# Performance work log

Hardware: AMD Instinct MI355X
Metric: run time of the kernel (lower is better)

## Reference

```python
import jax, jax.numpy as jnp
import numpy as np
import math

D_MODEL = 1024
N_HEADS = 16
D_K = D_MODEL // N_HEADS
D_FF = 4096
B, S = 4, 2048
EPS = 1e-5


def setup_inputs() -> dict:
    key = jax.random.key(0)
    ks = jax.random.split(key, 16)
    def xav(k, shape):
        fan_in, fan_out = shape[0], shape[1]
        lim = math.sqrt(6.0 / (fan_in + fan_out))
        return jax.random.uniform(k, shape, jnp.float32, -lim, lim)
    return {
        "query": jax.random.normal(ks[0], (B, S, D_MODEL), jnp.float32),
        "key": jax.random.normal(ks[1], (B, S, D_MODEL), jnp.float32),
        "values": jax.random.normal(ks[2], (B, S, D_MODEL), jnp.float32),
        # weights stored (in, out) so y = x @ W + b (transpose of torch layout)
        "Wk": xav(ks[3], (D_MODEL, D_MODEL)), "bk": jnp.zeros((D_MODEL,)),
        "Wv": xav(ks[4], (D_MODEL, D_MODEL)), "bv": jnp.zeros((D_MODEL,)),
        "Wout": xav(ks[5], (D_MODEL, D_MODEL)), "bout": jnp.zeros((D_MODEL,)),
        "gammas": jax.random.normal(ks[6], (N_HEADS, 1, 1), jnp.float32) * 0.5,
        "ln1_s": jnp.ones((D_MODEL,)), "ln1_b": jnp.zeros((D_MODEL,)),
        "W1": xav(ks[7], (D_MODEL, D_FF)), "b1": jnp.zeros((D_FF,)),
        "W2": xav(ks[8], (D_FF, D_MODEL)), "b2": jnp.zeros((D_MODEL,)),
        "ln2_s": jnp.ones((D_MODEL,)), "ln2_b": jnp.zeros((D_MODEL,)),
    }


def _layernorm(x, scale, bias):
    mu = jnp.mean(x, axis=-1, keepdims=True)
    var = jnp.mean((x - mu) ** 2, axis=-1, keepdims=True)
    return (x - mu) * jax.lax.rsqrt(var + EPS) * scale + bias


def reference(query, key, values, Wk, bk, Wv, bv, Wout, bout, gammas,
              ln1_s, ln1_b, W1, b1, W2, b2, ln2_s, ln2_b):
    bs, seqlen, _ = query.shape
    # NOTE: original code projects q with k_linear (shared weights) - kept faithful.
    q = (query @ Wk + bk).reshape(bs, seqlen, N_HEADS, D_K).transpose(0, 2, 1, 3)
    k = (key @ Wk + bk).reshape(bs, seqlen, N_HEADS, D_K).transpose(0, 2, 1, 3)
    v = (values @ Wv + bv).reshape(bs, seqlen, N_HEADS, D_K).transpose(0, 2, 1, 3)

    scores = jnp.einsum("bhqd,bhkd->bhqk", q, k) / math.sqrt(D_K)  # [B,H,S,S]

    idx = jnp.arange(seqlen)
    position_effect = jnp.abs(idx[None, :] - idx[:, None]).astype(jnp.float32) / 21.0  # [S,S]
    gamma = -jax.nn.softplus(gammas)  # [H,1,1]
    # exp(-pos * gamma) = exp(pos * softplus(gammas)), clamped to [1e-5, 1e5]
    total_effect = jnp.clip(jnp.exp(-position_effect[None, :, :] * gamma), 1e-5, 1e5)  # [H,S,S]
    scores = scores * total_effect[None]

    causal = jnp.tril(jnp.ones((seqlen, seqlen), dtype=bool))  # allowed positions
    scores = jnp.where(causal[None, None], scores, -1e32)
    att_weight = jax.nn.softmax(scores, axis=-1)  # dropout is identity (eval)

    ctx = jnp.einsum("bhqk,bhkd->bhqd", att_weight, v)
    concat = ctx.transpose(0, 2, 1, 3).reshape(bs, seqlen, D_MODEL)
    attn_out = concat @ Wout + bout

    x = _layernorm(query + attn_out, ln1_s, ln1_b)
    ffn = jax.nn.relu(x @ W1 + b1) @ W2 + b2
    x = _layernorm(x + ffn, ln2_s, ln2_b)
    return (x, att_weight)
```

## Files before the change

kernel.cpp:

```cpp
#include <hip/hip_runtime.h>
#include <math.h>

typedef unsigned short u16;
typedef float f32x4 __attribute__((ext_vector_type(4)));
typedef short s16x8 __attribute__((ext_vector_type(8)));

#define D_MODEL 1024
#define NH 16
#define DK 64
#define DFF 4096
#define BB 4
#define SS 2048
#define ROWS (BB*SS)
#define MiB 1048576ull
#define BHSZ 4194304ull
#define QKS  131072ull

static __device__ __forceinline__ float bf2f(u16 v){
  union{unsigned u; float f;} x; x.u = ((unsigned)v)<<16; return x.f;
}
static __device__ __forceinline__ u16 f2bf(float f){
  union{float f; unsigned u;} x; x.f=f;
  unsigned r = x.u + 0x7fffu + ((x.u>>16)&1u);
  return (u16)(r>>16);
}
static __device__ __forceinline__ double softplus64(float gf){
  double g = (double)gf;
  return (g > 0.0) ? g + log1p(exp(-g)) : log1p(exp(g));
}

__global__ __launch_bounds__(256) void twc(const float* __restrict__ in,
    u16* __restrict__ oh, u16* __restrict__ om, u16* __restrict__ ol, int R, int C){
  __shared__ float t[32][33];
  int c0 = blockIdx.x*32, r0 = blockIdx.y*32;
  int tx = threadIdx.x & 31, ty = threadIdx.x >> 5;
  for (int i=ty; i<32; i+=8) t[i][tx] = in[(size_t)(r0+i)*C + c0 + tx];
  __syncthreads();
  for (int i=ty; i<32; i+=8){
    float x = t[tx][i];
    u16 h = f2bf(x);
    size_t o = (size_t)(c0+i)*R + r0 + tx;
    oh[o] = h;
    if (om){
      float r1 = x - bf2f(h);
      u16 m = f2bf(r1);
      om[o] = m;
      if (ol){ float r2 = r1 - bf2f(m); ol[o] = f2bf(r2); }
    }
  }
}

__global__ __launch_bounds__(256) void copyf(float* __restrict__ dst,
                                             const float* __restrict__ src, long long n){
  long long i = (long long)blockIdx.x*256 + threadIdx.x;
  long long stride = (long long)gridDim.x*256;
  for (; i < n; i += stride) dst[i] = src[i];
}

__global__ __launch_bounds__(256) void gemm3(
    const float* __restrict__ A, const u16* __restrict__ Bh,
    const u16* __restrict__ Bm, const u16* __restrict__ Bl,
    const float* __restrict__ bias, int M, int N, int K, int kt, float* __restrict__ o)
{
  __shared__ u16 lAh[128*32], lAm[128*32], lAl[128*32];
  __shared__ u16 lBh[128*32], lBm[128*32], lBl[128*32];
  const int tid = threadIdx.x, wid = tid>>6, L = tid&63;
  const int m0 = blockIdx.y*128, n0 = blockIdx.x*128;
  const int wm = (wid>>1)*64, wn = (wid&1)*64;
  f32x4 acc[4][4] = {};
  const int srow = wid*32 + (L>>2);
  const int scol = (L&3)*8;
  for (int ktile=0; ktile<K; ktile+=32){
    s16x8 ah[2], am[2], al[2], vbh[2], vbm[2], vbl[2];
    #pragma unroll
    for (int rr=0; rr<2; rr++){
      const float* ap = &A[(size_t)(m0 + srow + rr*16)*K + ktile + scol];
      #pragma unroll
      for (int e=0;e<8;e++){
        float x = ap[e];
        u16 hh = f2bf(x); float r1 = x - bf2f(hh);
        u16 mm = f2bf(r1); float r2 = r1 - bf2f(mm);
        ah[rr][e] = (short)hh; am[rr][e] = (short)mm; al[rr][e] = (short)f2bf(r2);
      }
      const size_t bo = (size_t)(n0 + srow + rr*16)*K + ktile + scol;
      vbh[rr] = *(const s16x8*)&Bh[bo];
      vbm[rr] = *(const s16x8*)&Bm[bo];
      vbl[rr] = *(const s16x8*)&Bl[bo];
    }
    __syncthreads();
    #pragma unroll
    for (int rr=0; rr<2; rr++){
      const int ro = (srow + rr*16)*32 + scol;
      *(s16x8*)&lAh[ro] = ah[rr]; *(s16x8*)&lAm[ro] = am[rr]; *(s16x8*)&lAl[ro] = al[rr];
      *(s16x8*)&lBh[ro] = vbh[rr]; *(s16x8*)&lBm[ro] = vbm[rr]; *(s16x8*)&lBl[ro] = vbl[rr];
    }
    __syncthreads();
    const int lro = (L&15)*32 + (L>>4)*8;
    s16x8 afh[4], afm[4], afl[4], bfh[4], bfm[4], bfl[4];
    #pragma unroll
    for (int t=0;t<4;t++){
      afh[t] = *(const s16x8*)&lAh[(wm + t*16)*32 + lro];
      afm[t] = *(const s16x8*)&lAm[(wm + t*16)*32 + lro];
      afl[t] = *(const s16x8*)&lAl[(wm + t*16)*32 + lro];
      bfh[t] = *(const s16x8*)&lBh[(wn + t*16)*32 + lro];
      bfm[t] = *(const s16x8*)&lBm[(wn + t*16)*32 + lro];
      bfl[t] = *(const s16x8*)&lBl[(wn + t*16)*32 + lro];
    }
    #pragma unroll
    for (int mt=0;mt<4;mt++)
      #pragma unroll
      for (int nt=0;nt<4;nt++){
        f32x4 a2 = acc[mt][nt];
        a2 = __builtin_amdgcn_mfma_f32_16x16x32_bf16(afl[mt], bfh[nt], a2, 0,0,0);
        a2 = __builtin_amdgcn_mfma_f32_16x16x32_bf16(afm[mt], bfm[nt], a2, 0,0,0);
        a2 = __builtin_amdgcn_mfma_f32_16x16x32_bf16(afh[mt], bfl[nt], a2, 0,0,0);
        a2 = __builtin_amdgcn_mfma_f32_16x16x32_bf16(afm[mt], bfh[nt], a2, 0,0,0);
        a2 = __builtin_amdgcn_mfma_f32_16x16x32_bf16(afh[mt], bfm[nt], a2, 0,0,0);
        a2 = __builtin_amdgcn_mfma_f32_16x16x32_bf16(afh[mt], bfh[nt], a2, 0,0,0);
        acc[mt][nt] = a2;
      }
  }
  #pragma unroll
  for (int mt=0;mt<4;mt++)
    #pragma unroll
    for (int nt=0;nt<4;nt++){
      const int gn = n0 + wn + nt*16 + (L&15);
      const float bvv = bias[gn];
      const int gmb = m0 + wm + mt*16 + (L>>4)*4;
      const int h = gn>>6, d = gn&63;
      #pragma unroll
      for (int r=0;r<4;r++){
        const int gm = gmb + r, b = gm>>11, s = gm&2047;
        const float v = acc[mt][nt][r] + bvv;
        if (kt) o[((size_t)(b*NH+h)*DK + d)*SS + s] = v;
        else    o[((size_t)(b*NH+h)*SS + s)*DK + d] = v;
      }
    }
}

__global__ __launch_bounds__(256) void gemm2(
    const float* __restrict__ A, const u16* __restrict__ Bh, const u16* __restrict__ Bl,
    const float* __restrict__ bias, int M, int N, int K, int mode, float* __restrict__ o)
{
  __shared__ u16 lAh[128*32], lAl[128*32], lBh[128*32], lBl[128*32];
  const int tid = threadIdx.x, wid = tid>>6, L = tid&63;
  const int m0 = blockIdx.y*128, n0 = blockIdx.x*128;
  const int wm = (wid>>1)*64, wn = (wid&1)*64;
  f32x4 acc[4][4] = {};
  const int srow = wid*32 + (L>>2);
  const int scol = (L&3)*8;
  for (int kt=0; kt<K; kt+=32){
    s16x8 ah[2], al[2], vbh[2], vbl[2];
    #pragma unroll
    for (int rr=0; rr<2; rr++){
      const float* ap = &A[(size_t)(m0 + srow + rr*16)*K + kt + scol];
      #pragma unroll
      for (int e=0;e<8;e++){
        float x = ap[e];
        u16 hh = f2bf(x);
        ah[rr][e] = (short)hh;
        al[rr][e] = (short)f2bf(x - bf2f(hh));
      }
      const size_t bo = (size_t)(n0 + srow + rr*16)*K + kt + scol;
      vbh[rr] = *(const s16x8*)&Bh[bo];
      vbl[rr] = *(const s16x8*)&Bl[bo];
    }
    __syncthreads();
    #pragma unroll
    for (int rr=0; rr<2; rr++){
      const int ro = (srow + rr*16)*32 + scol;
      *(s16x8*)&lAh[ro] = ah[rr]; *(s16x8*)&lAl[ro] = al[rr];
      *(s16x8*)&lBh[ro] = vbh[rr]; *(s16x8*)&lBl[ro] = vbl[rr];
    }
    __syncthreads();
    const int lro = (L&15)*32 + (L>>4)*8;
    s16x8 afh[4], afl[4], bfh[4], bfl[4];
    #pragma unroll
    for (int t=0;t<4;t++){
      afh[t] = *(const s16x8*)&lAh[(wm + t*16)*32 + lro];
      afl[t] = *(const s16x8*)&lAl[(wm + t*16)*32 + lro];
      bfh[t] = *(const s16x8*)&lBh[(wn + t*16)*32 + lro];
      bfl[t] = *(const s16x8*)&lBl[(wn + t*16)*32 + lro];
    }
    #pragma unroll
    for (int mt=0;mt<4;mt++)
      #pragma unroll
      for (int nt=0;nt<4;nt++){
        f32x4 a2 = acc[mt][nt];
        a2 = __builtin_amdgcn_mfma_f32_16x16x32_bf16(afl[mt], bfh[nt], a2, 0,0,0);
        a2 = __builtin_amdgcn_mfma_f32_16x16x32_bf16(afh[mt], bfl[nt], a2, 0,0,0);
        a2 = __builtin_amdgcn_mfma_f32_16x16x32_bf16(afh[mt], bfh[nt], a2, 0,0,0);
        acc[mt][nt] = a2;
      }
  }
  #pragma unroll
  for (int mt=0;mt<4;mt++)
    #pragma unroll
    for (int nt=0;nt<4;nt++){
      const int gn = n0 + wn + nt*16 + (L&15);
      const float bvv = bias[gn];
      const int gmb = m0 + wm + mt*16 + (L>>4)*4;
      #pragma unroll
      for (int r=0;r<4;r++){
        const int gm = gmb + r;
        float v = acc[mt][nt][r] + bvv;
        if (mode==0)      o[(size_t)gm*N + gn] = v;
        else if (mode==1) o[(size_t)gm*N + gn] = fmaxf(v, 0.f);
        else {
          const int b = gm>>11, s = gm&2047, h = gn>>6, d = gn&63;
          o[((size_t)(b*NH+h)*SS + s)*DK + d] = v;
        }
      }
    }
}

__global__ __launch_bounds__(256) void attn_row(
  const float* __restrict__ q, const float* __restrict__ k, long long qs,
  int bh0, int row0,
  const float* __restrict__ vb, const float* __restrict__ gammas,
  float* __restrict__ att, float* __restrict__ ctx,
  int aw_lo, int aw_hi, int wc)
{
  __shared__ float  sqf[64][4];
  __shared__ float  p4[1024*4];
  __shared__ double red[4][4];
  __shared__ float  cpart[4][4][64];
  const int i0 = row0 + blockIdx.x*4;
  const int i3 = i0 + 3;
  const int bh = bh0 + blockIdx.y, h = bh&15, b = bh>>4;
  const int wa = (bh >= aw_lo) && (bh < aw_hi);
  const int t = threadIdx.x, wid = t>>6, L = t&63;
  const double c = softplus64(gammas[h]) * (1.0/21.0);

  {
    const int r = t>>6, d = t&63;
    sqf[d][r] = q[(size_t)blockIdx.y*qs + (size_t)(i0+r)*DK + d];
  }
  const double ce1   = exp(-c);
  const double er    = exp(c);
  const double tstep = exp(-1024.0 * c);
  double u0 = exp(c * (double)(i0 - 4*t));
  double err1 = er, err2 = er*er, err3 = err2*er;
  __syncthreads();

  const float* kb = k + (size_t)blockIdx.y*qs;
  double sv[4][8];
  double lmax[4] = {-1e300,-1e300,-1e300,-1e300};
  #pragma unroll
  for (int tile=0; tile<2; tile++){
    const int j0 = tile*1024 + 4*t;
    if (j0 <= i3){
      const float* kcol = kb + j0;
      double acc[4][4];
      #pragma unroll
      for (int r=0;r<4;r++)
        #pragma unroll
        for (int e=0;e<4;e++) acc[r][e] = 0.0;
      #pragma unroll 4
      for (int d=0; d<64; d++){
        f32x4 kv = *(const f32x4*)(kcol + (size_t)d*SS);
        f32x4 qv = *(const f32x4*)&sqf[d][0];
        const double k0=(double)kv[0], k1=(double)kv[1];
        const double k2=(double)kv[2], k3=(double)kv[3];
        #pragma unroll
        for (int r=0;r<4;r++){
          const double qd = (double)qv[r];
          acc[r][0] = fma(k0, qd, acc[r][0]);
          acc[r][1] = fma(k1, qd, acc[r][1]);
          acc[r][2] = fma(k2, qd, acc[r][2]);
          acc[r][3] = fma(k3, qd, acc[r][3]);
        }
      }
      #pragma unroll
      for (int r=0;r<4;r++){
        double uu = u0 * ((r==0)?1.0:(r==1)?err1:(r==2)?err2:err3);
        const int ir = i0 + r;
        #pragma unroll
        for (int e=0;e<4;e++){
          const double ef = ((uu < 1e5) ? uu : 1e5) * 0.125;
          const double s = (j0 + e <= ir) ? acc[r][e]*ef : -1e300;
          sv[r][tile*4+e] = s;
          lmax[r] = (lmax[r] > s) ? lmax[r] : s;
          uu *= ce1;
        }
      }
    }
    u0 *= tstep;
  }
  #pragma unroll
  for (int r=0;r<4;r++){
    double lm = lmax[r];
    #pragma unroll
    for (int m2=1;m2<64;m2<<=1){ double o2 = __shfl_xor(lm,m2,64); lm = (lm>o2)?lm:o2; }
    if (L==0) red[wid][r] = lm;
  }
  __syncthreads();
  double m[4];
  #pragma unroll
  for (int r=0;r<4;r++){
    double mm = red[0][r];
    mm = (mm>red[1][r])?mm:red[1][r];
    mm = (mm>red[2][r])?mm:red[2][r];
    mm = (mm>red[3][r])?mm:red[3][r];
    m[r] = mm;
  }
  __syncthreads();

  float ev[4][8];
  double lsum[4] = {0.0,0.0,0.0,0.0};
  #pragma unroll
  for (int tile=0; tile<2; tile++){
    const int j0 = tile*1024 + 4*t;
    if (j0 <= i3){
      #pragma unroll
      for (int r=0;r<4;r++)
        #pragma unroll
        for (int e=0;e<4;e++){
          float ex = expf((float)(sv[r][tile*4+e] - m[r]));
          ev[r][tile*4+e] = ex;
          lsum[r] += (double)ex;
        }
    }
  }
  #pragma unroll
  for (int r=0;r<4;r++){
    double ls = lsum[r];
    #pragma unroll
    for (int m2=1;m2<64;m2<<=1) ls += __shfl_xor(ls,m2,64);
    if (L==0) red[wid][r] = ls;
  }
  __syncthreads();
  float inv[4];
  #pragma unroll
  for (int r=0;r<4;r++)
    inv[r] = (float)(1.0 / (red[0][r]+red[1][r]+red[2][r]+red[3][r]));

  float ac0[4] = {0.f,0.f,0.f,0.f};
  float ac1[4] = {0.f,0.f,0.f,0.f};
  const int gg = t>>6, d = t&63;
  const float* vr = &vb[(size_t)bh*SS*DK + d];
  #pragma unroll
  for (int tile=0; tile<2; tile++){
    const int base = tile*1024;
    const int j0 = base + 4*t;
    if (wc){
      if (tile) __syncthreads();
      if (j0 <= i3){
        #pragma unroll
        for (int e=0;e<4;e++){
          f32x4 w;
          w[0] = ev[0][tile*4+e]*inv[0]; w[1] = ev[1][tile*4+e]*inv[1];
          w[2] = ev[2][tile*4+e]*inv[2]; w[3] = ev[3][tile*4+e]*inv[3];
          *(f32x4*)&p4[(4*t+e)*4] = w;
        }
      }
      __syncthreads();
    }
    if (wa){
      const int jj = 4*t;
      #pragma unroll
      for (int r=0;r<4;r++){
        const int ir = i0 + r;
        float* rb = &att[((size_t)bh*SS + ir)*SS + base];
        const float iv = inv[r];
        f32x4 o;
        o[0] = (base+jj   <= ir) ? ev[r][tile*4+0]*iv : 0.f;
        o[1] = (base+jj+1 <= ir) ? ev[r][tile*4+1]*iv : 0.f;
        o[2] = (base+jj+2 <= ir) ? ev[r][tile*4+2]*iv : 0.f;
        o[3] = (base+jj+3 <= ir) ? ev[r][tile*4+3]*iv : 0.f;
        *(f32x4*)&rb[jj] = o;
      }
    }
    if (wc){
      int hi = i3 - base; if (hi > 1023) hi = 1023;
      const float* vt = vr + (size_t)base*DK;
      int jj = gg;
      for (; jj+4 <= hi; jj += 8){
        const float v0 = vt[(size_t)jj*DK];
        const float v1 = vt[(size_t)(jj+4)*DK];
        f32x4 pa = *(const f32x4*)&p4[jj*4];
        f32x4 pb = *(const f32x4*)&p4[(jj+4)*4];
        #pragma unroll
        for (int r=0;r<4;r++){
          ac0[r] = fmaf(pa[r], v0, ac0[r]);
          ac1[r] = fmaf(pb[r], v1, ac1[r]);
        }
      }
      for (; jj <= hi; jj += 4){
        const float v0 = vt[(size_t)jj*DK];
        f32x4 pa = *(const f32x4*)&p4[jj*4];
        #pragma unroll
        for (int r=0;r<4;r++) ac0[r] = fmaf(pa[r], v0, ac0[r]);
      }
    }
  }
  if (wc){
    #pragma unroll
    for (int r=0;r<4;r++) cpart[r][gg][d] = ac0[r] + ac1[r];
    __syncthreads();
    {
      const int r = t>>6, dd = t&63;
      const float cc = cpart[r][0][dd]+cpart[r][1][dd]+cpart[r][2][dd]+cpart[r][3][dd];
      ctx[((size_t)(b*SS + (i0+r))*NH + h)*DK + dd] = cc;
    }
  }
}

__global__ __launch_bounds__(256) void attn_corner(
  const float* __restrict__ src, const float* __restrict__ gammas,
  float* __restrict__ att)
{
  __shared__ float lq[128*64];
  __shared__ float lk[128*64];
  const int t = threadIdx.x;
  for (int idx = t; idx < 128*64; idx += 256)
    lq[idx] = src[idx];
  for (int idx = t; idx < 64*128; idx += 256){
    const int d = idx >> 7, s = idx & 127;
    lk[s*64 + d] = src[QKS + (size_t)d*SS + s];
  }
  __syncthreads();
  const double sp = softplus64(gammas[15]);
  const int w = t>>6, L = t&63;
  for (int i = w; i < 128; i += 4){
    double s0 = -1e300, s1 = -1e300;
    if (L <= i){
      double a = 0.0;
      for (int d=0; d<64; d++) a = fma((double)lq[i*64+d], (double)lk[L*64+d], a);
      double eff = exp((double)(i-L)*(1.0/21.0)*sp); eff = (eff<1e5)?eff:1e5;
      s0 = a * 0.125 * eff;
    }
    if (64+L <= i){
      double a = 0.0;
      for (int d=0; d<64; d++) a = fma((double)lq[i*64+d], (double)lk[(64+L)*64+d], a);
      double eff = exp((double)(i-64-L)*(1.0/21.0)*sp); eff = (eff<1e5)?eff:1e5;
      s1 = a * 0.125 * eff;
    }
    double mx = (s0>s1)?s0:s1;
    #pragma unroll
    for (int m2=1;m2<64;m2<<=1){ double o2 = __shfl_xor(mx,m2,64); mx = (mx>o2)?mx:o2; }
    double e0 = (L<=i)    ? exp(s0-mx) : 0.0;
    double e1 = (64+L<=i) ? exp(s1-mx) : 0.0;
    double su = e0+e1;
    #pragma unroll
    for (int m2=1;m2<64;m2<<=1) su += __shfl_xor(su,m2,64);
    const double inv = 1.0/su;
    const float p0 = (float)(e0*inv), p1 = (float)(e1*inv);
    float* rb = &att[((size_t)63*SS + i)*SS];
    #pragma unroll
    for (int tt=0; tt<32; tt++)
      rb[tt*64+L] = (tt==0) ? p0 : (tt==1) ? p1 : 0.f;
  }
}

__global__ __launch_bounds__(256) void lnorm(
  const float* __restrict__ a, const float* __restrict__ b,
  const float* __restrict__ sc, const float* __restrict__ bi,
  float* __restrict__ out)
{
  __shared__ float red[4];
  const int row = blockIdx.x, tid = threadIdx.x, wid = tid>>6;
  const size_t rb = (size_t)row*D_MODEL;
  float x[4];
  #pragma unroll
  for (int i=0;i<4;i++){
    const int c = tid + i*256;
    x[i] = a[rb+c] + b[rb+c];
  }
  float s = x[0]+x[1]+x[2]+x[3];
  for (int m2=1;m2<64;m2<<=1) s += __shfl_xor(s,m2,64);
  if ((tid&63)==0) red[wid] = s;
  __syncthreads();
  const float mu = (red[0]+red[1]+red[2]+red[3]) * (1.0f/1024.0f);
  __syncthreads();
  float ss2 = 0.f;
  #pragma unroll
  for (int i=0;i<4;i++){ float d = x[i]-mu; ss2 += d*d; }
  for (int m2=1;m2<64;m2<<=1) ss2 += __shfl_xor(ss2,m2,64);
  if ((tid&63)==0) red[wid] = ss2;
  __syncthreads();
  const float var = (red[0]+red[1]+red[2]+red[3]) * (1.0f/1024.0f);
  const float inv = rsqrtf(var + 1e-5f);
  #pragma unroll
  for (int i=0;i<4;i++){
    const int c = tid + i*256;
    out[rb+c] = (x[i]-mu)*inv*sc[c] + bi[c];
  }
}

extern "C" void kernel_launch(void* const* d_in, const int* in_sizes, int n_in,
                              void* d_out, int out_size, void* d_ws, size_t ws_size,
                              hipStream_t stream)
{
  const float* query  = (const float*)d_in[0];
  const float* key    = (const float*)d_in[1];
  const float* values = (const float*)d_in[2];
  const float* Wk   = (const float*)d_in[3];
  const float* bk   = (const float*)d_in[4];
  const float* Wv   = (const float*)d_in[5];
  const float* bv   = (const float*)d_in[6];
  const float* Wout = (const float*)d_in[7];
  const float* bout = (const float*)d_in[8];
  const float* gammas = (const float*)d_in[9];
  const float* ln1s = (const float*)d_in[10];
  const float* ln1b = (const float*)d_in[11];
  const float* W1   = (const float*)d_in[12];
  const float* b1   = (const float*)d_in[13];
  const float* W2   = (const float*)d_in[14];
  const float* b2   = (const float*)d_in[15];
  const float* ln2s = (const float*)d_in[16];
  const float* ln2b = (const float*)d_in[17];

  float* outx = (float*)d_out;
  float* att  = outx + (size_t)ROWS*D_MODEL;

  const bool usews = (d_ws != nullptr) && (ws_size >= 240ull*MiB);
  char* sc = usews ? (char*)d_ws : (char*)att;
  u16* WkTh  = (u16*)(sc +  0*MiB);
  u16* WkTm  = (u16*)(sc +  2*MiB);
  u16* WkTl  = (u16*)(sc +  4*MiB);
  u16* WvTh  = (u16*)(sc +  6*MiB);
  u16* WvTl  = (u16*)(sc +  8*MiB);
  u16* WoTh  = (u16*)(sc + 10*MiB);
  u16* WoTl  = (u16*)(sc + 12*MiB);
  u16* W1Th  = (u16*)(sc + 14*MiB);
  u16* W1Tl  = (u16*)(sc + 22*MiB);
  u16* W2Th  = (u16*)(sc + 30*MiB);
  u16* W2Tl  = (u16*)(sc + 38*MiB);
  float* vbp  = (float*)(sc +  48*MiB);
  float* ctxb = (float*)(sc +  80*MiB);
  float* aof  = (float*)(sc +  48*MiB);
  float* x1f  = (float*)(sc +  80*MiB);
  float* hbuf = (float*)(sc + 112*MiB);
  float* fbuf = (float*)(sc + 144*MiB);
  float* QF = usews ? (float*)(sc + 176*MiB) : att + 60*BHSZ;
  float* KF = usews ? (float*)(sc + 208*MiB) : att + 62*BHSZ;
  float* D1 = att + 63*BHSZ + 2*(MiB/4)*4;
  float* D2 = att + 63*BHSZ;

  dim3 th(256);
  twc<<<dim3(32,32),  th, 0, stream>>>(Wk,   WkTh, WkTm, WkTl, 1024, 1024);
  twc<<<dim3(32,32),  th, 0, stream>>>(Wv,   WvTh, WvTl, nullptr, 1024, 1024);
  twc<<<dim3(32,32),  th, 0, stream>>>(Wout, WoTh, WoTl, nullptr, 1024, 1024);
  twc<<<dim3(128,32), th, 0, stream>>>(W1,   W1Th, W1Tl, nullptr, 1024, 4096);
  twc<<<dim3(32,128), th, 0, stream>>>(W2,   W2Th, W2Tl, nullptr, 4096, 1024);
  gemm3<<<dim3(8,64), th, 0, stream>>>(query, WkTh, WkTm, WkTl, bk, ROWS, 1024, 1024, 0, QF);
  gemm3<<<dim3(8,64), th, 0, stream>>>(key,   WkTh, WkTm, WkTl, bk, ROWS, 1024, 1024, 1, KF);
  gemm2<<<dim3(8,64), th, 0, stream>>>(values, WvTh, WvTl, bv, ROWS, 1024, 1024, 2, vbp);
  if (usews){
    attn_row<<<dim3(SS/4,64), th, 0, stream>>>(QF, KF, (long long)QKS, 0, 0,
                                               vbp, gammas, att, ctxb, 0, 64, 1);
  } else {
    attn_row<<<dim3(SS/4,64), th, 0, stream>>>(QF, KF, (long long)QKS, 0, 0,
                                               vbp, gammas, att, ctxb, 11, 60, 1);
  }
  gemm2<<<dim3(8,64),  th, 0, stream>>>(ctxb, WoTh, WoTl, bout, ROWS, 1024, 1024, 0, aof);
  lnorm<<<dim3(ROWS), th, 0, stream>>>(query, aof, ln1s, ln1b, x1f);
  for (int c = 0; c < 4; ++c){
    gemm2<<<dim3(32,16), th, 0, stream>>>(x1f + (size_t)c*2048*1024, W1Th, W1Tl, b1,
                                          2048, 4096, 1024, 1, hbuf);
    gemm2<<<dim3(8,16),  th, 0, stream>>>(hbuf, W2Th, W2Tl, b2,
                                          2048, 1024, 4096, 0, fbuf + (size_t)c*2048*1024);
  }
  lnorm<<<dim3(ROWS), th, 0, stream>>>(x1f, fbuf, ln2s, ln2b, outx);
  if (!usews){
    attn_row<<<dim3(SS/4,11), th, 0, stream>>>(QF, KF, (long long)QKS, 0, 0,
                                               vbp, gammas, att, ctxb, 0, 64, 0);
    copyf<<<dim3(512), th, 0, stream>>>(D1,            QF + 60*QKS, 4*(long long)QKS);
    copyf<<<dim3(512), th, 0, stream>>>(D1 + 4*QKS,    KF + 60*QKS, 4*(long long)QKS);
    attn_row<<<dim3(SS/4,3), th, 0, stream>>>(D1, D1 + 4*QKS, (long long)QKS, 60, 0,
                                              vbp, gammas, att, ctxb, 0, 64, 0);
    attn_row<<<dim3(128,1), th, 0, stream>>>(D1 + 3*QKS, D1 + 7*QKS, 0ll, 63, 1536,
                                             vbp, gammas, att, ctxb, 0, 64, 0);
    copyf<<<dim3(128), th, 0, stream>>>(D2,        D1 + 3*QKS, (long long)QKS);
    copyf<<<dim3(128), th, 0, stream>>>(D2 + QKS,  D1 + 7*QKS, (long long)QKS);
    attn_row<<<dim3(352,1), th, 0, stream>>>(D2, D2 + QKS, 0ll, 63, 128,
                                             vbp, gammas, att, ctxb, 0, 64, 0);
    attn_corner<<<dim3(1), th, 0, stream>>>(D2, gammas, att);
  }
}
```

Baseline: 4.379 ms.

## Split attention into score/softmax kernel and MFMA-based P·V GEMM

When the workspace path is used, the fused attention-row kernel is replaced by two stages. The first computes causal scores, decay and softmax and writes the attention weights. The second re-reads those weights and multiplies them by V on MFMA units, using a split-bf16 (hi/lo, three-product) scheme. V is now written transposed as bf16 hi/lo pairs so the GEMM can load it directly. This moves the P·V product from scalar code onto matrix cores, at the cost of an extra full read of the large attention matrix and some precision loss from the bf16 split.

```diff
diff --git a/kernel.cpp b/kernel.cpp
--- a/kernel.cpp
+++ b/kernel.cpp
@@ -206,10 +206,234 @@
         float v = acc[mt][nt][r] + bvv;
         if (mode==0)      o[(size_t)gm*N + gn] = v;
         else if (mode==1) o[(size_t)gm*N + gn] = fmaxf(v, 0.f);
-        else {
+        else if (mode==3){
+          const int b = gm>>11, s = gm&2047, h = gn>>6, d = gn&63;
+          u16* vh = (u16*)o;
+          u16* vl = vh + 8388608ull;
+          const size_t off = ((size_t)(b*NH+h)*DK + d)*SS + s;
+          const u16 hh = f2bf(v);
+          vh[off] = hh;
+          vl[off] = f2bf(v - bf2f(hh));
+        } else {
           const int b = gm>>11, s = gm&2047, h = gn>>6, d = gn&63;
           o[((size_t)(b*NH+h)*SS + s)*DK + d] = v;
         }
+      }
+    }
+}
+
+__global__ __launch_bounds__(256) void attn_sc(
+  const float* __restrict__ q, const float* __restrict__ k,
+  const float* __restrict__ gammas, float* __restrict__ att)
+{
+  __shared__ float  sqf[64][4];
+  __shared__ double red[4][4];
+  const int i0 = blockIdx.x*4;
+  const int i3 = i0 + 3;
+  const int bh = blockIdx.y, h = bh&15;
+  const int t = threadIdx.x, wid = t>>6, L = t&63;
+  const double c = softplus64(gammas[h]) * (1.0/21.0);
+
+  {
+    const int r = t>>6, d = t&63;
+    sqf[d][r] = q[(size_t)bh*QKS + (size_t)(i0+r)*DK + d];
+  }
+  const double ce1   = exp(-c);
+  const double er    = exp(c);
+  const double tstep = exp(-1024.0 * c);
+  double u0 = exp(c * (double)(i0 - 4*t));
+  double err1 = er, err2 = er*er, err3 = err2*er;
+  __syncthreads();
+
+  const float* kb = k + (size_t)bh*QKS;
+  double sv[4][8];
+  double lmax[4] = {-1e300,-1e300,-1e300,-1e300};
+  #pragma unroll
+  for (int tile=0; tile<2; tile++){
+    const int j0 = tile*1024 + 4*t;
+    if (j0 <= i3){
+      const float* kcol = kb + j0;
+      double acc[4][4];
+      #pragma unroll
+      for (int r=0;r<4;r++)
+        #pragma unroll
+        for (int e=0;e<4;e++) acc[r][e] = 0.0;
+      #pragma unroll 4
+      for (int d=0; d<64; d++){
+        f32x4 kv = *(const f32x4*)(kcol + (size_t)d*SS);
+        f32x4 qv = *(const f32x4*)&sqf[d][0];
+        const double k0=(double)kv[0], k1=(double)kv[1];
+        const double k2=(double)kv[2], k3=(double)kv[3];
+        #pragma unroll
+        for (int r=0;r<4;r++){
+          const double qd = (double)qv[r];
+          acc[r][0] = fma(k0, qd, acc[r][0]);
+          acc[r][1] = fma(k1, qd, acc[r][1]);
+          acc[r][2] = fma(k2, qd, acc[r][2]);
+          acc[r][3] = fma(k3, qd, acc[r][3]);
+        }
+      }
+      #pragma unroll
+      for (int r=0;r<4;r++){
+        double uu = u0 * ((r==0)?1.0:(r==1)?err1:(r==2)?err2:err3);
+        const int ir = i0 + r;
+        #pragma unroll
+        for (int e=0;e<4;e++){
+          const double ef = ((uu < 1e5) ? uu : 1e5) * 0.125;
+          const double s = (j0 + e <= ir) ? acc[r][e]*ef : -1e300;
+          sv[r][tile*4+e] = s;
+          lmax[r] = (lmax[r] > s) ? lmax[r] : s;
+          uu *= ce1;
+        }
+      }
+    }
+    u0 *= tstep;
+  }
+  #pragma unroll
+  for (int r=0;r<4;r++){
+    double lm = lmax[r];
+    #pragma unroll
+    for (int m2=1;m2<64;m2<<=1){ double o2 = __shfl_xor(lm,m2,64); lm = (lm>o2)?lm:o2; }
+    if (L==0) red[wid][r] = lm;
+  }
+  __syncthreads();
+  double m[4];
+  #pragma unroll
+  for (int r=0;r<4;r++){
+    double mm = red[0][r];
+    mm = (mm>red[1][r])?mm:red[1][r];
+    mm = (mm>red[2][r])?mm:red[2][r];
+    mm = (mm>red[3][r])?mm:red[3][r];
+    m[r] = mm;
+  }
+  __syncthreads();
+
+  float ev[4][8];
+  double lsum[4] = {0.0,0.0,0.0,0.0};
+  #pragma unroll
+  for (int tile=0; tile<2; tile++){
+    const int j0 = tile*1024 + 4*t;
+    if (j0 <= i3){
+      #pragma unroll
+      for (int r=0;r<4;r++)
+        #pragma unroll
+        for (int e=0;e<4;e++){
+          float ex = expf((float)(sv[r][tile*4+e] - m[r]));
+          ev[r][tile*4+e] = ex;
+          lsum[r] += (double)ex;
+        }
+    }
+  }
+  #pragma unroll
+  for (int r=0;r<4;r++){
+    double ls = lsum[r];
+    #pragma unroll
+    for (int m2=1;m2<64;m2<<=1) ls += __shfl_xor(ls,m2,64);
+    if (L==0) red[wid][r] = ls;
+  }
+  __syncthreads();
+  float inv[4];
+  #pragma unroll
+  for (int r=0;r<4;r++)
+    inv[r] = (float)(1.0 / (red[0][r]+red[1][r]+red[2][r]+red[3][r]));
+
+  #pragma unroll
+  for (int tile=0; tile<2; tile++){
+    const int base = tile*1024;
+    const int jj = 4*t;
+    #pragma unroll
+    for (int r=0;r<4;r++){
+      const int ir = i0 + r;
+      float* rb = &att[((size_t)bh*SS + ir)*SS + base];
+      const float iv = inv[r];
+      f32x4 o;
+      o[0] = (base+jj   <= ir) ? ev[r][tile*4+0]*iv : 0.f;
+      o[1] = (base+jj+1 <= ir) ? ev[r][tile*4+1]*iv : 0.f;
+      o[2] = (base+jj+2 <= ir) ? ev[r][tile*4+2]*iv : 0.f;
+      o[3] = (base+jj+3 <= ir) ? ev[r][tile*4+3]*iv : 0.f;
+      *(f32x4*)&rb[jj] = o;
+    }
+  }
+}
+
+__global__ __launch_bounds__(256) void pvg(
+  const float* __restrict__ att, const u16* __restrict__ Vh, const u16* __restrict__ Vl,
+  float* __restrict__ ctx)
+{
+  __shared__ u16 lAh[128*32], lAl[128*32], lBh[64*32], lBl[64*32];
+  const int tid = threadIdx.x, wid = tid>>6, L = tid&63;
+  const int bh = blockIdx.y, m0 = blockIdx.x*128;
+  const int b = bh>>4, h = bh&15;
+  const float* A  = att + (size_t)bh*BHSZ;
+  const u16*  Bhp = Vh + (size_t)bh*DK*SS;
+  const u16*  Blp = Vl + (size_t)bh*DK*SS;
+  const int wm = wid*32;
+  f32x4 acc[2][4] = {};
+  const int srow = wid*32 + (L>>2);
+  const int scol = (L&3)*8;
+  const int db   = tid>>2;
+  const int scb  = (tid&3)*8;
+  const int Klim = m0 + 128;
+  for (int kt=0; kt<Klim; kt+=32){
+    s16x8 ah[2], al[2], vh8, vl8;
+    #pragma unroll
+    for (int rr=0; rr<2; rr++){
+      const float* ap = &A[(size_t)(m0 + srow + rr*16)*SS + kt + scol];
+      #pragma unroll
+      for (int e=0;e<8;e++){
+        float x = ap[e];
+        u16 hh = f2bf(x);
+        ah[rr][e] = (short)hh;
+        al[rr][e] = (short)f2bf(x - bf2f(hh));
+      }
+    }
+    {
+      const size_t bo = (size_t)db*SS + kt + scb;
+      vh8 = *(const s16x8*)&Bhp[bo];
+      vl8 = *(const s16x8*)&Blp[bo];
+    }
+    __syncthreads();
+    #pragma unroll
+    for (int rr=0; rr<2; rr++){
+      const int ro = (srow + rr*16)*32 + scol;
+      *(s16x8*)&lAh[ro] = ah[rr]; *(s16x8*)&lAl[ro] = al[rr];
+    }
+    *(s16x8*)&lBh[db*32 + scb] = vh8;
+    *(s16x8*)&lBl[db*32 + scb] = vl8;
+    __syncthreads();
+    const int lro = (L&15)*32 + (L>>4)*8;
+    s16x8 afh[2], afl[2], bfh[4], bfl[4];
+    #pragma unroll
+    for (int mt=0;mt<2;mt++){
+      afh[mt] = *(const s16x8*)&lAh[(wm + mt*16)*32 + lro];
+      afl[mt] = *(const s16x8*)&lAl[(wm + mt*16)*32 + lro];
+    }
+    #pragma unroll
+    for (int nt=0;nt<4;nt++){
+      bfh[nt] = *(const s16x8*)&lBh[(nt*16)*32 + lro];
+      bfl[nt] = *(const s16x8*)&lBl[(nt*16)*32 + lro];
+    }
+    #pragma unroll
+    for (int mt=0;mt<2;mt++)
+      #pragma unroll
+      for (int nt=0;nt<4;nt++){
+        f32x4 a2 = acc[mt][nt];
+        a2 = __builtin_amdgcn_mfma_f32_16x16x32_bf16(afl[mt], bfh[nt], a2, 0,0,0);
+        a2 = __builtin_amdgcn_mfma_f32_16x16x32_bf16(afh[mt], bfl[nt], a2, 0,0,0);
+        a2 = __builtin_amdgcn_mfma_f32_16x16x32_bf16(afh[mt], bfh[nt], a2, 0,0,0);
+        acc[mt][nt] = a2;
+      }
+  }
+  #pragma unroll
+  for (int mt=0;mt<2;mt++)
+    #pragma unroll
+    for (int nt=0;nt<4;nt++){
+      const int d = nt*16 + (L&15);
+      const int gmb = m0 + wm + mt*16 + (L>>4)*4;
+      #pragma unroll
+      for (int r=0;r<4;r++){
+        const int s = gmb + r;
+        ctx[((size_t)(b*SS + s)*NH + h)*DK + d] = acc[mt][nt][r];
       }
     }
 }
@@ -546,11 +770,13 @@
   twc<<<dim3(32,128), th, 0, stream>>>(W2,   W2Th, W2Tl, nullptr, 4096, 1024);
   gemm3<<<dim3(8,64), th, 0, stream>>>(query, WkTh, WkTm, WkTl, bk, ROWS, 1024, 1024, 0, QF);
   gemm3<<<dim3(8,64), th, 0, stream>>>(key,   WkTh, WkTm, WkTl, bk, ROWS, 1024, 1024, 1, KF);
-  gemm2<<<dim3(8,64), th, 0, stream>>>(values, WvTh, WvTl, bv, ROWS, 1024, 1024, 2, vbp);
   if (usews){
-    attn_row<<<dim3(SS/4,64), th, 0, stream>>>(QF, KF, (long long)QKS, 0, 0,
-                                               vbp, gammas, att, ctxb, 0, 64, 1);
+    gemm2<<<dim3(8,64), th, 0, stream>>>(values, WvTh, WvTl, bv, ROWS, 1024, 1024, 3, vbp);
+    attn_sc<<<dim3(SS/4,64), th, 0, stream>>>(QF, KF, gammas, att);
+    pvg<<<dim3(16,64), th, 0, stream>>>(att, (const u16*)vbp,
+                                        (const u16*)vbp + 8388608ull, ctxb);
   } else {
+    gemm2<<<dim3(8,64), th, 0, stream>>>(values, WvTh, WvTl, bv, ROWS, 1024, 1024, 2, vbp);
     attn_row<<<dim3(SS/4,64), th, 0, stream>>>(QF, KF, (long long)QKS, 0, 0,
                                                vbp, gammas, att, ctxb, 11, 60, 1);
   }
```

New measurement: 3.739 ms. 14.6% less time.
